# Optimization experiments

Measured on AMD Instinct MI355X. Metric: run time of the kernel, lower is better.

The kernel has to match this reference:

```python
import jax, jax.numpy as jnp
import numpy as np

TEMPERATURE = 8.0  # sqrt(d_k=64)
NEG_FILL = -1000.0


def setup_inputs() -> dict:
    key = jax.random.key(0)
    k1, k2, k3, k4 = jax.random.split(key, 4)
    B, Lq, Lk, D = 16, 2048, 2048, 64
    q = jax.random.normal(k1, (B, Lq, D), dtype=jnp.float32)
    k = jax.random.normal(k2, (B, Lk, D), dtype=jnp.float32)
    v = jax.random.normal(k3, (B, Lk, D), dtype=jnp.float32)
    pad_mask = jax.random.randint(k4, (B, Lk), 0, 2).astype(bool)
    return {"q": q, "k": k, "v": v, "pad_mask": pad_mask}


def reference(q, k, v, pad_mask):
    # scores: [B, Lq, Lk]
    attn = jnp.einsum('bqd,bkd->bqk', q, k) / TEMPERATURE
    # mask padded keys (broadcast over query dim, like pad_mask.unsqueeze(1))
    attn = jnp.where(pad_mask[:, None, :], NEG_FILL, attn)
    attn = jax.nn.softmax(attn, axis=-1)
    # dropout is identity in eval / p=0
    output = jnp.einsum('bqk,bkd->bqd', attn, v)
    return output, attn
```

## Files before the change

kernel.cpp:

```cpp
#include <hip/hip_runtime.h>
#include <hip/hip_bf16.h>

#define BB 16
#define LL 2048
#define DD 64

typedef __attribute__((ext_vector_type(8))) short short8t;
typedef __attribute__((ext_vector_type(4))) float f32x4;
typedef __attribute__((ext_vector_type(4))) unsigned short ushort4t;

__device__ __forceinline__ unsigned short f2bf(float x) {
  union { float f; unsigned int u; } c; c.f = x;
  unsigned int u = c.u;
  u += 0x7fffu + ((u >> 16) & 1u);
  return (unsigned short)(u >> 16);
}

__global__ void prep(const float* __restrict__ q, const float* __restrict__ k,
                     const float* __restrict__ v,
                     unsigned short* __restrict__ Qb, unsigned short* __restrict__ Kb,
                     unsigned short* __restrict__ VT) {
  __shared__ unsigned short t[64][66];
  int bid = blockIdx.x;
  if (bid < 4096) {
    const float* in = (bid < 2048) ? q : k;
    unsigned short* outp = (bid < 2048) ? Qb : Kb;
    int i = (bid & 2047) * 1024 + threadIdx.x * 4;
    float4 v4 = *(const float4*)(in + i);
    ushort4t o;
    o.x = f2bf(v4.x); o.y = f2bf(v4.y); o.z = f2bf(v4.z); o.w = f2bf(v4.w);
    *(ushort4t*)(outp + i) = o;
  } else {
    int vb = bid - 4096;
    int b = vb >> 5, j0 = (vb & 31) * 64;
    const float* src = v + ((size_t)b * LL + j0) * DD;
#pragma unroll
    for (int i = 0; i < 16; ++i) {
      int lin = i * 256 + threadIdx.x;
      int j = lin >> 6, d = lin & 63;
      t[j][d] = f2bf(src[lin]);
    }
    __syncthreads();
    unsigned short* dst = VT + (size_t)b * DD * LL;
#pragma unroll
    for (int i = 0; i < 16; ++i) {
      int lin = i * 256 + threadIdx.x;
      int d = lin >> 6, j = lin & 63;
      dst[(size_t)d * LL + j0 + j] = t[j][d];
    }
  }
}

__device__ __forceinline__ void async_cp16(const unsigned short* src, unsigned short* dst_lds) {
  __builtin_amdgcn_global_load_lds(
      (const __attribute__((address_space(1))) unsigned int*)src,
      (__attribute__((address_space(3))) unsigned int*)dst_lds, 16, 0, 0);
}

__global__ void __launch_bounds__(256, 2)
attn_main(const unsigned short* __restrict__ Qb, const unsigned short* __restrict__ Kb,
          const unsigned short* __restrict__ VTb, const int* __restrict__ mask,
          float* __restrict__ out, float* __restrict__ attn) {
  __shared__ __align__(16) unsigned short TB[40960];

  const int tid = threadIdx.x;
  const int w = tid >> 6;
  const int l = tid & 63;
  const int l15 = l & 15;
  const int g = l >> 4;

  const int swzb = (blockIdx.x & 7) * 64 + (blockIdx.x >> 3);
  const int b = swzb >> 5;
  const int q0 = (swzb & 31) << 6;

  unsigned short* KT0 = TB;
  unsigned short* KT1 = TB + 8192;
  unsigned short* VTt = TB + 16384;
  float* PFw = (float*)(TB + 24576) + w * 2048;

  const unsigned short* Kbb = Kb + (size_t)b * LL * DD;
  const unsigned short* VTbb = VTb + (size_t)b * DD * LL;
  const int* maskb = mask + b * LL;

  auto stageK = [&](int t, unsigned short* KB) {
    int k0 = (t & 15) * 128;
    const unsigned short* gs = Kbb + (size_t)k0 * DD;
#pragma unroll
    for (int i2 = 0; i2 < 4; ++i2) {
      int row = i2 * 32 + w * 8 + (l >> 3);
      int ce = ((l & 7) * 8) ^ ((row & 3) << 4);
      async_cp16(gs + row * 64 + ce, KB + (i2 * 32 + w * 8) * 64);
    }
  };
  auto stageV = [&](int t) {
    int k0 = (t & 15) * 128;
#pragma unroll
    for (int i2 = 0; i2 < 4; ++i2) {
      int row = i2 * 16 + w * 4 + (l >> 4);
      int ce = ((l & 15) * 8) ^ ((row & 3) << 4);
      async_cp16(VTbb + (size_t)row * LL + k0 + ce, VTt + (i2 * 16 + w * 4) * 128);
    }
  };
  auto loadMask = [&](int t, int* mk) {
    int k0 = (t & 15) * 128;
#pragma unroll
    for (int ni = 0; ni < 8; ++ni) mk[ni] = maskb[k0 + 16 * ni + l15];
  };

  short8t qf[2];
  {
    const unsigned short* qbase = Qb + ((size_t)b * LL + q0 + 16 * w + l15) * DD + 8 * g;
    qf[0] = *(const short8t*)(qbase);
    qf[1] = *(const short8t*)(qbase + 32);
  }

  float ls[4] = {0.f, 0.f, 0.f, 0.f};
  int mkA[8], mkB[8];

  auto stepA = [&](int t, const unsigned short* KBc, unsigned short* KBn,
                   const int* mkc, int* mkn) {
    asm volatile("s_waitcnt vmcnt(0)" ::: "memory");
    __syncthreads();
    loadMask(t + 1, mkn);
    stageK(t + 1, KBn);
    __builtin_amdgcn_sched_barrier(0);
    short8t kf[8][2];
#pragma unroll
    for (int ni = 0; ni < 8; ++ni)
#pragma unroll
      for (int h = 0; h < 2; ++h)
        kf[ni][h] = *(const short8t*)(KBc + (16 * ni + l15) * 64 + ((32 * h + 8 * g) ^ ((l15 & 3) << 4)));
    f32x4 sacc[8] = {};
    __builtin_amdgcn_s_setprio(1);
#pragma unroll
    for (int ni = 0; ni < 8; ++ni)
#pragma unroll
      for (int h = 0; h < 2; ++h)
        sacc[ni] = __builtin_amdgcn_mfma_f32_16x16x32_bf16(qf[h], kf[ni][h], sacc[ni], 0, 0, 0);
    __builtin_amdgcn_s_setprio(0);
#pragma unroll
    for (int ni = 0; ni < 8; ++ni) {
      int mk = mkc[ni];
#pragma unroll
      for (int r = 0; r < 4; ++r)
        ls[r] += mk ? 0.f : __expf(sacc[ni][r] * 0.125f);
    }
  };

  stageK(0, KT0);
  loadMask(0, mkA);
  for (int jj = 0; jj < 8; ++jj) {
    stepA(2 * jj, KT0, KT1, mkA, mkB);
    stepA(2 * jj + 1, KT1, KT0, mkB, mkA);
  }

  float rinv_[4];
#pragma unroll
  for (int r = 0; r < 4; ++r) {
    float s = ls[r];
    s += __shfl_xor(s, 1);
    s += __shfl_xor(s, 2);
    s += __shfl_xor(s, 4);
    s += __shfl_xor(s, 8);
    rinv_[r] = 1.0f / s;
  }

  f32x4 oacc[4] = {};
  const size_t abase0 = (size_t)(b * LL + q0 + 16 * w) * LL;

  auto stepB = [&](int t, bool first, const unsigned short* KBc, unsigned short* KBn,
                   const int* mkc, int* mkn) {
    if (first) { asm volatile("s_waitcnt vmcnt(0)" ::: "memory"); }
    else       { asm volatile("s_waitcnt vmcnt(8)" ::: "memory"); }
    __syncthreads();
    const int k0 = (t & 15) * 128;

    short8t vf[4][4];
#pragma unroll
    for (int kk = 0; kk < 4; ++kk)
#pragma unroll
      for (int ni = 0; ni < 4; ++ni)
        vf[kk][ni] = *(const short8t*)(VTt + (16 * ni + l15) * 128 + ((32 * kk + 8 * g) ^ ((l15 & 3) << 4)));
    asm volatile("s_waitcnt lgkmcnt(0)" ::: "memory");
    __builtin_amdgcn_sched_barrier(0);
    __syncthreads();

    loadMask(t + 1, mkn);
    stageK(t + 1, KBn);
    stageV(t + 1);
    __builtin_amdgcn_sched_barrier(0);

    short8t kf[8][2];
#pragma unroll
    for (int ni = 0; ni < 8; ++ni)
#pragma unroll
      for (int h = 0; h < 2; ++h)
        kf[ni][h] = *(const short8t*)(KBc + (16 * ni + l15) * 64 + ((32 * h + 8 * g) ^ ((l15 & 3) << 4)));
    f32x4 sacc[8] = {};
    __builtin_amdgcn_s_setprio(1);
#pragma unroll
    for (int ni = 0; ni < 8; ++ni)
#pragma unroll
      for (int h = 0; h < 2; ++h)
        sacc[ni] = __builtin_amdgcn_mfma_f32_16x16x32_bf16(qf[h], kf[ni][h], sacc[ni], 0, 0, 0);
    __builtin_amdgcn_s_setprio(0);

#pragma unroll
    for (int ni = 0; ni < 8; ++ni) {
      int mk = mkc[ni];
#pragma unroll
      for (int r = 0; r < 4; ++r) {
        float p = mk ? 0.f : __expf(sacc[ni][r] * 0.125f) * rinv_[r];
        PFw[(4 * g + r) * 128 + ((16 * ni + l15) ^ ((g & 1) << 4))] = p;
      }
    }
    asm volatile("s_waitcnt lgkmcnt(0)" ::: "memory");
    __builtin_amdgcn_sched_barrier(0);

#pragma unroll
    for (int it = 0; it < 8; ++it) {
      int row = l >> 2;
      int cb = (l & 3) * 4 + 16 * it;
      f32x4 pv = *(const f32x4*)(PFw + row * 128 + (cb ^ (((row >> 2) & 1) << 4)));
      *(f32x4*)(attn + abase0 + (size_t)row * LL + k0 + cb) = pv;
    }

    short8t pfr[4];
#pragma unroll
    for (int kk = 0; kk < 4; ++kk) {
      const float* src = PFw + l15 * 128 + ((32 * kk + 8 * g) ^ (((l15 >> 2) & 1) << 4));
      f32x4 pa = *(const f32x4*)(src);
      f32x4 pb = *(const f32x4*)(src + 4);
      short8t f;
      f[0] = (short)f2bf(pa[0]); f[1] = (short)f2bf(pa[1]);
      f[2] = (short)f2bf(pa[2]); f[3] = (short)f2bf(pa[3]);
      f[4] = (short)f2bf(pb[0]); f[5] = (short)f2bf(pb[1]);
      f[6] = (short)f2bf(pb[2]); f[7] = (short)f2bf(pb[3]);
      pfr[kk] = f;
    }
    __builtin_amdgcn_s_setprio(1);
#pragma unroll
    for (int kk = 0; kk < 4; ++kk)
#pragma unroll
      for (int ni = 0; ni < 4; ++ni)
        oacc[ni] = __builtin_amdgcn_mfma_f32_16x16x32_bf16(pfr[kk], vf[kk][ni], oacc[ni], 0, 0, 0);
    __builtin_amdgcn_s_setprio(0);
  };

  stageV(0);
  stepB(0, true, KT0, KT1, mkA, mkB);
  for (int jj = 0; jj < 7; ++jj) {
    stepB(2 * jj + 1, false, KT1, KT0, mkB, mkA);
    stepB(2 * jj + 2, false, KT0, KT1, mkA, mkB);
  }
  stepB(15, false, KT1, KT0, mkB, mkA);

  asm volatile("s_waitcnt vmcnt(0)" ::: "memory");

#pragma unroll
  for (int ni = 0; ni < 4; ++ni)
#pragma unroll
    for (int r = 0; r < 4; ++r)
      out[(size_t)(b * LL + q0 + 16 * w + 4 * g + r) * DD + 16 * ni + l15] = oacc[ni][r];
}

extern "C" void kernel_launch(void* const* d_in, const int* in_sizes, int n_in,
                              void* d_out, int out_size, void* d_ws, size_t ws_size,
                              hipStream_t stream) {
  const float* q = (const float*)d_in[0];
  const float* k = (const float*)d_in[1];
  const float* v = (const float*)d_in[2];
  const int* pm = (const int*)d_in[3];

  float* out = (float*)d_out;
  float* attn = out + (size_t)BB * LL * DD;

  unsigned short* Qb = (unsigned short*)d_ws;
  unsigned short* Kb = Qb + (size_t)BB * LL * DD;
  unsigned short* VT = Kb + (size_t)BB * LL * DD;

  prep<<<4608, 256, 0, stream>>>(q, k, v, Qb, Kb, VT);
  attn_main<<<512, 256, 0, stream>>>(Qb, Kb, VT, pm, out, attn);
}
```

Baseline: 103.9 us.

## Split key range across waves per 16-query block with exp2 bias softmax

Restructures the main kernel so each 128-thread block handles 16 queries and its two waves each cover half of the keys. Each wave streams its own 32-key K/V tiles with no block-wide barriers, and the two halves' row sums and output partials are combined through LDS. The scale factor log2(e)/8 is folded into Q in the prep kernel, and the mask becomes a precomputed additive bias of -180, so the kernel calls exp2f with no select. This trades far more blocks and smaller tiles (more K/V reloads, more launch granularity) for higher occupancy and less synchronization. The -180 bias approximates the -1000 fill, which holds only while unmasked scores stay bounded.

```diff
diff --git a/kernel.cpp b/kernel.cpp
--- a/kernel.cpp
+++ b/kernel.cpp
@@ -4,6 +4,7 @@
 #define BB 16
 #define LL 2048
 #define DD 64
+#define QSCALE 0.1803368801111602f
 
 typedef __attribute__((ext_vector_type(8))) short short8t;
 typedef __attribute__((ext_vector_type(4))) float f32x4;
@@ -17,20 +18,23 @@
 }
 
 __global__ void prep(const float* __restrict__ q, const float* __restrict__ k,
-                     const float* __restrict__ v,
+                     const float* __restrict__ v, const int* __restrict__ pm,
                      unsigned short* __restrict__ Qb, unsigned short* __restrict__ Kb,
-                     unsigned short* __restrict__ VT) {
+                     unsigned short* __restrict__ VT, float* __restrict__ biasF) {
   __shared__ unsigned short t[64][66];
   int bid = blockIdx.x;
   if (bid < 4096) {
-    const float* in = (bid < 2048) ? q : k;
-    unsigned short* outp = (bid < 2048) ? Qb : Kb;
+    bool isQ = bid < 2048;
+    const float* in = isQ ? q : k;
+    unsigned short* outp = isQ ? Qb : Kb;
+    float sc = isQ ? QSCALE : 1.0f;
     int i = (bid & 2047) * 1024 + threadIdx.x * 4;
     float4 v4 = *(const float4*)(in + i);
     ushort4t o;
-    o.x = f2bf(v4.x); o.y = f2bf(v4.y); o.z = f2bf(v4.z); o.w = f2bf(v4.w);
+    o.x = f2bf(v4.x * sc); o.y = f2bf(v4.y * sc);
+    o.z = f2bf(v4.z * sc); o.w = f2bf(v4.w * sc);
     *(ushort4t*)(outp + i) = o;
-  } else {
+  } else if (bid < 4608) {
     int vb = bid - 4096;
     int b = vb >> 5, j0 = (vb & 31) * 64;
     const float* src = v + ((size_t)b * LL + j0) * DD;
@@ -48,6 +52,13 @@
       int d = lin >> 6, j = lin & 63;
       dst[(size_t)d * LL + j0 + j] = t[j][d];
     }
+  } else {
+    int idx = (bid - 4608) * 1024 + threadIdx.x * 4;
+    int4 m4 = *(const int4*)(pm + idx);
+    float4 o;
+    o.x = m4.x ? -180.f : 0.f; o.y = m4.y ? -180.f : 0.f;
+    o.z = m4.z ? -180.f : 0.f; o.w = m4.w ? -180.f : 0.f;
+    *(float4*)(biasF + idx) = o;
   }
 }
 
@@ -57,11 +68,11 @@
       (__attribute__((address_space(3))) unsigned int*)dst_lds, 16, 0, 0);
 }
 
-__global__ void __launch_bounds__(256, 2)
+__global__ void __launch_bounds__(128, 4)
 attn_main(const unsigned short* __restrict__ Qb, const unsigned short* __restrict__ Kb,
-          const unsigned short* __restrict__ VTb, const int* __restrict__ mask,
+          const unsigned short* __restrict__ VTb, const float* __restrict__ biasF,
           float* __restrict__ out, float* __restrict__ attn) {
-  __shared__ __align__(16) unsigned short TB[40960];
+  __shared__ __align__(16) unsigned short TB[2][5120];
 
   const int tid = threadIdx.x;
   const int w = tid >> 6;
@@ -69,199 +80,211 @@
   const int l15 = l & 15;
   const int g = l >> 4;
 
-  const int swzb = (blockIdx.x & 7) * 64 + (blockIdx.x >> 3);
-  const int b = swzb >> 5;
-  const int q0 = (swzb & 31) << 6;
-
-  unsigned short* KT0 = TB;
-  unsigned short* KT1 = TB + 8192;
-  unsigned short* VTt = TB + 16384;
-  float* PFw = (float*)(TB + 24576) + w * 2048;
+  const int swz = (blockIdx.x & 7) * 256 + (blockIdx.x >> 3);
+  const int b = swz >> 7;
+  const int q0 = (swz & 127) << 4;
+
+  unsigned short* KB = &TB[w][0];
+  unsigned short* VB = &TB[w][2048];
+  float* PF = (float*)&TB[w][4096];
 
   const unsigned short* Kbb = Kb + (size_t)b * LL * DD;
   const unsigned short* VTbb = VTb + (size_t)b * DD * LL;
-  const int* maskb = mask + b * LL;
-
-  auto stageK = [&](int t, unsigned short* KB) {
-    int k0 = (t & 15) * 128;
-    const unsigned short* gs = Kbb + (size_t)k0 * DD;
+  const float* biasb = biasF + b * LL;
+
+  auto loadK = [&](int t) {
+    const unsigned short* gs = Kbb + (size_t)(t * 32) * DD;
 #pragma unroll
     for (int i2 = 0; i2 < 4; ++i2) {
-      int row = i2 * 32 + w * 8 + (l >> 3);
-      int ce = ((l & 7) * 8) ^ ((row & 3) << 4);
-      async_cp16(gs + row * 64 + ce, KB + (i2 * 32 + w * 8) * 64);
+      int row = i2 * 8 + (l >> 3);
+      int ce = (l & 7) * 8;
+      async_cp16(gs + row * 64 + (ce ^ ((row & 3) << 4)), KB + i2 * 512);
     }
   };
-  auto stageV = [&](int t) {
-    int k0 = (t & 15) * 128;
+  auto loadV = [&](int t) {
+    const int k0 = t * 32;
 #pragma unroll
     for (int i2 = 0; i2 < 4; ++i2) {
-      int row = i2 * 16 + w * 4 + (l >> 4);
-      int ce = ((l & 15) * 8) ^ ((row & 3) << 4);
-      async_cp16(VTbb + (size_t)row * LL + k0 + ce, VTt + (i2 * 16 + w * 4) * 128);
-    }
-  };
-  auto loadMask = [&](int t, int* mk) {
-    int k0 = (t & 15) * 128;
-#pragma unroll
-    for (int ni = 0; ni < 8; ++ni) mk[ni] = maskb[k0 + 16 * ni + l15];
+      int row = i2 * 16 + (l >> 2);
+      int ce = (l & 3) * 8;
+      async_cp16(VTbb + (size_t)row * LL + k0 + (ce ^ ((row & 1) << 4)), VB + i2 * 512);
+    }
   };
 
   short8t qf[2];
   {
-    const unsigned short* qbase = Qb + ((size_t)b * LL + q0 + 16 * w + l15) * DD + 8 * g;
+    const unsigned short* qbase = Qb + ((size_t)b * LL + q0 + l15) * DD + 8 * g;
     qf[0] = *(const short8t*)(qbase);
     qf[1] = *(const short8t*)(qbase + 32);
   }
 
+  const int tA = w * 32;
+
   float ls[4] = {0.f, 0.f, 0.f, 0.f};
-  int mkA[8], mkB[8];
-
-  auto stepA = [&](int t, const unsigned short* KBc, unsigned short* KBn,
-                   const int* mkc, int* mkn) {
+  {
+    loadK(tA);
+    float b0c = biasb[tA * 32 + l15], b1c = biasb[tA * 32 + 16 + l15];
     asm volatile("s_waitcnt vmcnt(0)" ::: "memory");
+    for (int j = 0; j < 32; ++j) {
+      short8t kf[2][2];
+#pragma unroll
+      for (int ni = 0; ni < 2; ++ni)
+#pragma unroll
+        for (int h = 0; h < 2; ++h)
+          kf[ni][h] = *(const short8t*)(KB + (16 * ni + l15) * 64 + ((32 * h + 8 * g) ^ ((l15 & 3) << 4)));
+      asm volatile("s_waitcnt lgkmcnt(0)" ::: "memory");
+      __builtin_amdgcn_sched_barrier(0);
+      int tn = tA + ((j + 1) & 31);
+      loadK(tn);
+      float nb0 = biasb[tn * 32 + l15], nb1 = biasb[tn * 32 + 16 + l15];
+
+      f32x4 sacc[2] = {};
+      __builtin_amdgcn_s_setprio(1);
+#pragma unroll
+      for (int ni = 0; ni < 2; ++ni)
+#pragma unroll
+        for (int h = 0; h < 2; ++h)
+          sacc[ni] = __builtin_amdgcn_mfma_f32_16x16x32_bf16(qf[h], kf[ni][h], sacc[ni], 0, 0, 0);
+      __builtin_amdgcn_s_setprio(0);
+#pragma unroll
+      for (int ni = 0; ni < 2; ++ni) {
+        float bc = ni ? b1c : b0c;
+#pragma unroll
+        for (int r = 0; r < 4; ++r)
+          ls[r] += exp2f(sacc[ni][r] + bc);
+      }
+      asm volatile("s_waitcnt vmcnt(0)" ::: "memory");
+      __builtin_amdgcn_sched_barrier(0);
+      b0c = nb0; b1c = nb1;
+    }
+  }
+
+  float rinv_[4];
+  {
+#pragma unroll
+    for (int r = 0; r < 4; ++r) {
+      float s = ls[r];
+      s += __shfl_xor(s, 1);
+      s += __shfl_xor(s, 2);
+      s += __shfl_xor(s, 4);
+      s += __shfl_xor(s, 8);
+      ls[r] = s;
+    }
+    float* exch = (float*)&TB[0][4096];
+    if (l15 == 0) {
+#pragma unroll
+      for (int r = 0; r < 4; ++r) exch[w * 16 + 4 * g + r] = ls[r];
+    }
     __syncthreads();
-    loadMask(t + 1, mkn);
-    stageK(t + 1, KBn);
-    __builtin_amdgcn_sched_barrier(0);
-    short8t kf[8][2];
-#pragma unroll
-    for (int ni = 0; ni < 8; ++ni)
-#pragma unroll
-      for (int h = 0; h < 2; ++h)
-        kf[ni][h] = *(const short8t*)(KBc + (16 * ni + l15) * 64 + ((32 * h + 8 * g) ^ ((l15 & 3) << 4)));
-    f32x4 sacc[8] = {};
-    __builtin_amdgcn_s_setprio(1);
-#pragma unroll
-    for (int ni = 0; ni < 8; ++ni)
-#pragma unroll
-      for (int h = 0; h < 2; ++h)
-        sacc[ni] = __builtin_amdgcn_mfma_f32_16x16x32_bf16(qf[h], kf[ni][h], sacc[ni], 0, 0, 0);
-    __builtin_amdgcn_s_setprio(0);
-#pragma unroll
-    for (int ni = 0; ni < 8; ++ni) {
-      int mk = mkc[ni];
+#pragma unroll
+    for (int r = 0; r < 4; ++r)
+      rinv_[r] = 1.0f / (exch[4 * g + r] + exch[16 + 4 * g + r]);
+    __syncthreads();
+  }
+
+  f32x4 oacc[4] = {};
+  const size_t abase = (size_t)(b * LL + q0);
+  {
+    loadK(tA);
+    loadV(tA);
+    float b0c = biasb[tA * 32 + l15], b1c = biasb[tA * 32 + 16 + l15];
+    asm volatile("s_waitcnt vmcnt(0)" ::: "memory");
+    for (int j = 0; j < 32; ++j) {
+      const int t = tA + j;
+      const int k0 = t * 32;
+      short8t kf[2][2], vf[4];
+#pragma unroll
+      for (int ni = 0; ni < 2; ++ni)
+#pragma unroll
+        for (int h = 0; h < 2; ++h)
+          kf[ni][h] = *(const short8t*)(KB + (16 * ni + l15) * 64 + ((32 * h + 8 * g) ^ ((l15 & 3) << 4)));
+#pragma unroll
+      for (int ni = 0; ni < 4; ++ni)
+        vf[ni] = *(const short8t*)(VB + (16 * ni + l15) * 32 + ((8 * g) ^ ((l & 1) << 4)));
+      asm volatile("s_waitcnt lgkmcnt(0)" ::: "memory");
+      __builtin_amdgcn_sched_barrier(0);
+
+      int tn = tA + ((j + 1) & 31);
+      loadK(tn);
+      loadV(tn);
+      float nb0 = biasb[tn * 32 + l15], nb1 = biasb[tn * 32 + 16 + l15];
+
+      f32x4 sacc[2] = {};
+      __builtin_amdgcn_s_setprio(1);
+#pragma unroll
+      for (int ni = 0; ni < 2; ++ni)
+#pragma unroll
+        for (int h = 0; h < 2; ++h)
+          sacc[ni] = __builtin_amdgcn_mfma_f32_16x16x32_bf16(qf[h], kf[ni][h], sacc[ni], 0, 0, 0);
+      __builtin_amdgcn_s_setprio(0);
+
+#pragma unroll
+      for (int ni = 0; ni < 2; ++ni) {
+        float bc = ni ? b1c : b0c;
+#pragma unroll
+        for (int r = 0; r < 4; ++r) {
+          float p = exp2f(sacc[ni][r] + bc) * rinv_[r];
+          PF[(4 * g + r) * 32 + ((16 * ni + l15) ^ (r << 3) ^ ((g & 1) << 4))] = p;
+        }
+      }
+
+      {
+        int row = l >> 2;
+        int c0 = (l & 3) * 8;
+        int key = ((row & 3) << 3) ^ ((row & 4) << 2);
+        const float* src = PF + row * 32 + (c0 ^ key);
+        f32x4 s0 = *(const f32x4*)(src);
+        f32x4 s1 = *(const f32x4*)(src + 4);
+        float* dst = attn + (abase + row) * LL + k0 + c0;
+        *(f32x4*)(dst) = s0;
+        *(f32x4*)(dst + 4) = s1;
+      }
+
+      short8t pfr;
+      {
+        int key = ((l15 & 3) << 3) ^ ((l15 & 4) << 2);
+        const float* src = PF + l15 * 32 + ((8 * g) ^ key);
+        f32x4 pa = *(const f32x4*)(src);
+        f32x4 pb = *(const f32x4*)(src + 4);
+        short8t f;
+        f[0] = (short)f2bf(pa[0]); f[1] = (short)f2bf(pa[1]);
+        f[2] = (short)f2bf(pa[2]); f[3] = (short)f2bf(pa[3]);
+        f[4] = (short)f2bf(pb[0]); f[5] = (short)f2bf(pb[1]);
+        f[6] = (short)f2bf(pb[2]); f[7] = (short)f2bf(pb[3]);
+        pfr = f;
+      }
+      __builtin_amdgcn_s_setprio(1);
+#pragma unroll
+      for (int ni = 0; ni < 4; ++ni)
+        oacc[ni] = __builtin_amdgcn_mfma_f32_16x16x32_bf16(pfr, vf[ni], oacc[ni], 0, 0, 0);
+      __builtin_amdgcn_s_setprio(0);
+
+      asm volatile("s_waitcnt vmcnt(2)" ::: "memory");
+      __builtin_amdgcn_sched_barrier(0);
+      b0c = nb0; b1c = nb1;
+    }
+  }
+
+  asm volatile("s_waitcnt vmcnt(0)" ::: "memory");
+
+  __syncthreads();
+  float* Oex = (float*)&TB[1][0];
+  if (w == 1) {
+#pragma unroll
+    for (int ni = 0; ni < 4; ++ni)
 #pragma unroll
       for (int r = 0; r < 4; ++r)
-        ls[r] += mk ? 0.f : __expf(sacc[ni][r] * 0.125f);
-    }
-  };
-
-  stageK(0, KT0);
-  loadMask(0, mkA);
-  for (int jj = 0; jj < 8; ++jj) {
-    stepA(2 * jj, KT0, KT1, mkA, mkB);
-    stepA(2 * jj + 1, KT1, KT0, mkB, mkA);
-  }
-
-  float rinv_[4];
-#pragma unroll
-  for (int r = 0; r < 4; ++r) {
-    float s = ls[r];
-    s += __shfl_xor(s, 1);
-    s += __shfl_xor(s, 2);
-    s += __shfl_xor(s, 4);
-    s += __shfl_xor(s, 8);
-    rinv_[r] = 1.0f / s;
-  }
-
-  f32x4 oacc[4] = {};
-  const size_t abase0 = (size_t)(b * LL + q0 + 16 * w) * LL;
-
-  auto stepB = [&](int t, bool first, const unsigned short* KBc, unsigned short* KBn,
-                   const int* mkc, int* mkn) {
-    if (first) { asm volatile("s_waitcnt vmcnt(0)" ::: "memory"); }
-    else       { asm volatile("s_waitcnt vmcnt(8)" ::: "memory"); }
-    __syncthreads();
-    const int k0 = (t & 15) * 128;
-
-    short8t vf[4][4];
-#pragma unroll
-    for (int kk = 0; kk < 4; ++kk)
-#pragma unroll
-      for (int ni = 0; ni < 4; ++ni)
-        vf[kk][ni] = *(const short8t*)(VTt + (16 * ni + l15) * 128 + ((32 * kk + 8 * g) ^ ((l15 & 3) << 4)));
-    asm volatile("s_waitcnt lgkmcnt(0)" ::: "memory");
-    __builtin_amdgcn_sched_barrier(0);
-    __syncthreads();
-
-    loadMask(t + 1, mkn);
-    stageK(t + 1, KBn);
-    stageV(t + 1);
-    __builtin_amdgcn_sched_barrier(0);
-
-    short8t kf[8][2];
-#pragma unroll
-    for (int ni = 0; ni < 8; ++ni)
-#pragma unroll
-      for (int h = 0; h < 2; ++h)
-        kf[ni][h] = *(const short8t*)(KBc + (16 * ni + l15) * 64 + ((32 * h + 8 * g) ^ ((l15 & 3) << 4)));
-    f32x4 sacc[8] = {};
-    __builtin_amdgcn_s_setprio(1);
-#pragma unroll
-    for (int ni = 0; ni < 8; ++ni)
-#pragma unroll
-      for (int h = 0; h < 2; ++h)
-        sacc[ni] = __builtin_amdgcn_mfma_f32_16x16x32_bf16(qf[h], kf[ni][h], sacc[ni], 0, 0, 0);
-    __builtin_amdgcn_s_setprio(0);
-
-#pragma unroll
-    for (int ni = 0; ni < 8; ++ni) {
-      int mk = mkc[ni];
-#pragma unroll
-      for (int r = 0; r < 4; ++r) {
-        float p = mk ? 0.f : __expf(sacc[ni][r] * 0.125f) * rinv_[r];
-        PFw[(4 * g + r) * 128 + ((16 * ni + l15) ^ ((g & 1) << 4))] = p;
-      }
-    }
-    asm volatile("s_waitcnt lgkmcnt(0)" ::: "memory");
-    __builtin_amdgcn_sched_barrier(0);
-
-#pragma unroll
-    for (int it = 0; it < 8; ++it) {
-      int row = l >> 2;
-      int cb = (l & 3) * 4 + 16 * it;
-      f32x4 pv = *(const f32x4*)(PFw + row * 128 + (cb ^ (((row >> 2) & 1) << 4)));
-      *(f32x4*)(attn + abase0 + (size_t)row * LL + k0 + cb) = pv;
-    }
-
-    short8t pfr[4];
-#pragma unroll
-    for (int kk = 0; kk < 4; ++kk) {
-      const float* src = PFw + l15 * 128 + ((32 * kk + 8 * g) ^ (((l15 >> 2) & 1) << 4));
-      f32x4 pa = *(const f32x4*)(src);
-      f32x4 pb = *(const f32x4*)(src + 4);
-      short8t f;
-      f[0] = (short)f2bf(pa[0]); f[1] = (short)f2bf(pa[1]);
-      f[2] = (short)f2bf(pa[2]); f[3] = (short)f2bf(pa[3]);
-      f[4] = (short)f2bf(pb[0]); f[5] = (short)f2bf(pb[1]);
-      f[6] = (short)f2bf(pb[2]); f[7] = (short)f2bf(pb[3]);
-      pfr[kk] = f;
-    }
-    __builtin_amdgcn_s_setprio(1);
-#pragma unroll
-    for (int kk = 0; kk < 4; ++kk)
-#pragma unroll
-      for (int ni = 0; ni < 4; ++ni)
-        oacc[ni] = __builtin_amdgcn_mfma_f32_16x16x32_bf16(pfr[kk], vf[kk][ni], oacc[ni], 0, 0, 0);
-    __builtin_amdgcn_s_setprio(0);
-  };
-
-  stageV(0);
-  stepB(0, true, KT0, KT1, mkA, mkB);
-  for (int jj = 0; jj < 7; ++jj) {
-    stepB(2 * jj + 1, false, KT1, KT0, mkB, mkA);
-    stepB(2 * jj + 2, false, KT0, KT1, mkA, mkB);
-  }
-  stepB(15, false, KT1, KT0, mkB, mkA);
-
-  asm volatile("s_waitcnt vmcnt(0)" ::: "memory");
-
-#pragma unroll
-  for (int ni = 0; ni < 4; ++ni)
-#pragma unroll
-    for (int r = 0; r < 4; ++r)
-      out[(size_t)(b * LL + q0 + 16 * w + 4 * g + r) * DD + 16 * ni + l15] = oacc[ni][r];
+        Oex[(4 * g + r) * 64 + 16 * ni + l15] = oacc[ni][r];
+  }
+  __syncthreads();
+  if (w == 0) {
+#pragma unroll
+    for (int ni = 0; ni < 4; ++ni)
+#pragma unroll
+      for (int r = 0; r < 4; ++r)
+        out[(abase + 4 * g + r) * DD + 16 * ni + l15] =
+            oacc[ni][r] + Oex[(4 * g + r) * 64 + 16 * ni + l15];
+  }
 }
 
 extern "C" void kernel_launch(void* const* d_in, const int* in_sizes, int n_in,
@@ -278,7 +301,8 @@
   unsigned short* Qb = (unsigned short*)d_ws;
   unsigned short* Kb = Qb + (size_t)BB * LL * DD;
   unsigned short* VT = Kb + (size_t)BB * LL * DD;
-
-  prep<<<4608, 256, 0, stream>>>(q, k, v, Qb, Kb, VT);
-  attn_main<<<512, 256, 0, stream>>>(Qb, Kb, VT, pm, out, attn);
-}
+  float* biasF = (float*)(VT + (size_t)BB * LL * DD);
+
+  prep<<<4640, 256, 0, stream>>>(q, k, v, pm, Qb, Kb, VT, biasF);
+  attn_main<<<2048, 128, 0, stream>>>(Qb, Kb, VT, biasF, out, attn);
+}
```

Result: slower. 121.5 us (+16.9%).
